# Optimization experiments

Hardware: AMD Instinct MI355X
Metric: run time of the kernel (lower is better)

The kernel has to match this reference:

```python
import jax, jax.numpy as jnp
import numpy as np

N_MEL = 80
ATTN = 512
PRENET = 256
RNN = 1024
B, T = 32, 800


def setup_inputs() -> dict:
    key = jax.random.key(0)
    ks = jax.random.split(key, 10)
    s = lambda fan_in: 1.0 / np.sqrt(fan_in)
    return {
        "memory": jax.random.normal(ks[0], (B, T, ATTN), jnp.float32),
        "y_mels": jax.random.normal(ks[1], (B, T, N_MEL), jnp.float32),
        # Prenet: two bias-free linears with ReLU
        "prenet_w1": jax.random.uniform(ks[2], (PRENET, N_MEL), jnp.float32, -s(N_MEL), s(N_MEL)),
        "prenet_w2": jax.random.uniform(ks[3], (PRENET, PRENET), jnp.float32, -s(PRENET), s(PRENET)),
        # LSTM (1 layer): input dim = PRENET + ATTN = 768, gate order i,f,g,o
        "w_ih": jax.random.uniform(ks[4], (4 * RNN, PRENET + ATTN), jnp.float32, -s(RNN), s(RNN)),
        "w_hh": jax.random.uniform(ks[5], (4 * RNN, RNN), jnp.float32, -s(RNN), s(RNN)),
        "b_ih": jax.random.uniform(ks[6], (4 * RNN,), jnp.float32, -s(RNN), s(RNN)),
        "b_hh": jax.random.uniform(ks[7], (4 * RNN,), jnp.float32, -s(RNN), s(RNN)),
        # Linear projection: (RNN + ATTN) -> N_MEL, with bias
        "proj_w": jax.random.uniform(ks[8], (N_MEL, RNN + ATTN), jnp.float32, -s(RNN + ATTN), s(RNN + ATTN)),
        "proj_b": jax.random.uniform(ks[9], (N_MEL,), jnp.float32, -s(RNN + ATTN), s(RNN + ATTN)),
    }


def _decoder_fwd(memory, y_mels, prenet_w1, prenet_w2, w_ih, w_hh, b_ih, b_hh, proj_w, proj_b):
    b, t, _ = memory.shape
    # teacher-forced previous frames: step j consumes zeros (j=0) or y_mels[:, j-1]
    prev = jnp.concatenate([jnp.zeros((b, 1, N_MEL), memory.dtype), y_mels[:, : t - 1]], axis=1)  # [B,T,80]
    # prenet (eval mode: dropout off; double relu == relu)
    h = jax.nn.relu(jnp.einsum("btm,pm->btp", prev, prenet_w1))
    h = jax.nn.relu(jnp.einsum("btp,qp->btq", h, prenet_w2))  # [B,T,256]
    x = jnp.concatenate([h, memory], axis=-1)  # [B,T,768]
    # precompute input-to-gate contributions for all steps
    gates_in = jnp.einsum("btd,gd->tbg", x, w_ih) + (b_ih + b_hh)  # [T,B,4H]

    def step(carry, g_in):
        hh, cc = carry
        gates = g_in + hh @ w_hh.T  # [B,4H]
        i, f_, g, o = jnp.split(gates, 4, axis=-1)
        cc = jax.nn.sigmoid(f_) * cc + jax.nn.sigmoid(i) * jnp.tanh(g)
        hh = jax.nn.sigmoid(o) * jnp.tanh(cc)
        return (hh, cc), hh

    init = (jnp.zeros((b, RNN), memory.dtype), jnp.zeros((b, RNN), memory.dtype))
    _, hs = jax.lax.scan(step, init, gates_in)  # [T,B,H]
    hs = jnp.transpose(hs, (1, 0, 2))  # [B,T,H]
    out = jnp.concatenate([hs, memory], axis=-1)  # [B,T,H+ATTN]
    mel = jnp.einsum("btd,md->btm", out, proj_w) + proj_b  # [B,T,80]
    return mel.reshape(b, -1, N_MEL)


def reference(memory, y_mels, prenet_w1, prenet_w2, w_ih, w_hh, b_ih, b_hh, proj_w, proj_b):
    return _decoder_fwd(memory, y_mels, prenet_w1, prenet_w2, w_ih, w_hh, b_ih, b_hh, proj_w, proj_b)
```

## Files before the change

### kernel.cpp

```cpp
#include <hip/hip_runtime.h>
#include <hip/hip_bf16.h>

typedef unsigned short u16;
typedef unsigned int u32;
typedef unsigned long long u64;
typedef __attribute__((ext_vector_type(8))) short short8;
typedef __attribute__((ext_vector_type(4))) float f32x4;
typedef __attribute__((ext_vector_type(4))) u32 u32x4;

#define ROWS 25600

__device__ __forceinline__ u16 f2bf(float f){
  u32 x = __builtin_bit_cast(u32, f);
  u32 r = (x + 0x7FFFu + ((x >> 16) & 1u)) >> 16;
  return (u16)r;
}
__device__ __forceinline__ float bf2f(u16 h){
  return __builtin_bit_cast(float, ((u32)h) << 16);
}
__device__ __forceinline__ float sigf(float x){
  x = fminf(fmaxf(x, -30.f), 30.f);
  return 1.f / (1.f + __expf(-x));
}
__device__ __forceinline__ float tanh_(float x){
  x = fminf(fmaxf(x, -15.f), 15.f);
  float e = __expf(-2.f * x);
  return (1.f - e) / (1.f + e);
}


__global__ void initk(u32* wflags, u32* pflags, u16* hb){
  int i = blockIdx.x * blockDim.x + threadIdx.x;
  int stride = blockDim.x * gridDim.x;
  for (int j = i; j < 64 * 32; j += stride) wflags[j] = 0;
  for (int j = i; j < 192 * 32; j += stride) pflags[j] = 0;
  for (int j = i; j < 2 * 32 * 1024; j += stride) hb[j] = 0;
}

__global__ void sentinel_fill(float* out, int n, float val){
  for (int i = blockIdx.x * blockDim.x + threadIdx.x; i < n;
       i += blockDim.x * gridDim.x)
    out[i] = val;
}

__global__ void prep_prev(const float* __restrict__ ym, u16* __restrict__ prevp){
  int idx = blockIdx.x * blockDim.x + threadIdx.x;
  if (idx >= ROWS * 96) return;
  int r = idx / 96, c = idx - r * 96;
  int b = r / 800, t = r - b * 800;
  float v = 0.f;
  if (c < 80 && t > 0) v = ym[(u64)(b * 800 + (t - 1)) * 80 + c];
  prevp[idx] = f2bf(v);
}

__global__ void prep_w(const float* __restrict__ w1, const float* __restrict__ w2,
                       const float* __restrict__ wih, const float* __restrict__ pw,
                       const float* __restrict__ bih, const float* __restrict__ bhh,
                       const float* __restrict__ whh,
                       u16* __restrict__ w1p, u16* __restrict__ w2b,
                       u16* __restrict__ wihb, u16* __restrict__ projp,
                       float* __restrict__ bsum, u16* __restrict__ whhb){
  int idx = blockIdx.x * blockDim.x + threadIdx.x;
  const int n1 = 256 * 96, n2 = 256 * 256, n3 = 4096 * 768, n4 = 128 * 1536, n5 = 4096;
  const int n6 = 4096 * 1024;
  if (idx < n1){
    int r = idx / 96, c = idx - r * 96;
    w1p[idx] = (c < 80) ? f2bf(w1[r * 80 + c]) : (u16)0;
  } else if ((idx -= n1) < n2){
    w2b[idx] = f2bf(w2[idx]);
  } else if ((idx -= n2) < n3){
    wihb[idx] = f2bf(wih[idx]);
  } else if ((idx -= n3) < n4){
    int r = idx / 1536;
    projp[idx] = (r < 80) ? f2bf(pw[idx]) : (u16)0;
  } else if ((idx -= n4) < n5){
    bsum[idx] = bih[idx] + bhh[idx];
  } else if ((idx -= n5) < n6){
    whhb[idx] = f2bf(whh[idx]);
  }
}


template<int RELU, int OUTF32, int HASBIAS, int AMAP, int SPLIT>
__global__ __launch_bounds__(256, 2) void gemm_tn(
    const u16* __restrict__ A, const float* __restrict__ A2,
    const u16* __restrict__ W, void* __restrict__ Cv,
    const float* __restrict__ bias,
    int M, int K, int lda, int lda2, int ldw, int ldc, int nmax,
    int ksplit, int t0)
{
  __shared__ __align__(16) u16 As[128 * 32];
  __shared__ __align__(16) u16 Ws[128 * 32];
  const int tid = threadIdx.x;
  const int lane = tid & 63;
  const int wv = tid >> 6;
  const int wr = wv & 1, wc = wv >> 1;
  const int mtiles = M >> 7;
  const int ntiles = gridDim.x / mtiles;
  int bm, bn;
  if (mtiles & 7){
    bm = blockIdx.x % mtiles;
    bn = blockIdx.x / mtiles;
  } else {
    int per = 8 * ntiles;
    int g = blockIdx.x / per, rem = blockIdx.x % per;
    bm = g * 8 + (rem & 7);
    bn = rem >> 3;
  }
  const int m0 = bm << 7, n0 = bn << 7;
  const int KT = K >> 5;

  f32x4 acc[4][4] = {};

  const int r0 = tid >> 2, c0 = tid & 3;
  const int r1 = r0 + 64;
  const u16* Wb = W + (u64)n0 * ldw;
  const int ws0 = r0 * 32 + ((c0 ^ ((r0 >> 1) & 3)) << 3);
  const int ws1 = r1 * 32 + ((c0 ^ ((r1 >> 1) & 3)) << 3);

  auto rowmap = [&](int r) -> int {
    int gr = m0 + r;
    if (AMAP) return (gr & 31) * 800 + t0 + (gr >> 5);
    return gr;
  };
  const u64 ab0 = (u64)rowmap(r0) * lda;
  const u64 ab1 = (u64)rowmap(r1) * lda;
  const u64 af0 = SPLIT ? (u64)rowmap(r0) * lda2 : 0;
  const u64 af1 = SPLIT ? (u64)rowmap(r1) * lda2 : 0;

  auto aload = [&](u64 rb, u64 rf, int k) -> uint4 {
    if (SPLIT && k >= ksplit){
      const float* p = A2 + rf + (k - ksplit);
      const float4 a = *(const float4*)p;
      const float4 b = *(const float4*)(p + 4);
      uint4 r;
      r.x = (u32)f2bf(a.x) | ((u32)f2bf(a.y) << 16);
      r.y = (u32)f2bf(a.z) | ((u32)f2bf(a.w) << 16);
      r.z = (u32)f2bf(b.x) | ((u32)f2bf(b.y) << 16);
      r.w = (u32)f2bf(b.z) | ((u32)f2bf(b.w) << 16);
      return r;
    }
    return *(const uint4*)(A + rb + k);
  };

  uint4 ra0 = aload(ab0, af0, c0 * 8);
  uint4 ra1 = aload(ab1, af1, c0 * 8);
  uint4 rw0 = *(const uint4*)(Wb + r0 * ldw + c0 * 8);
  uint4 rw1 = *(const uint4*)(Wb + r1 * ldw + c0 * 8);

  const int r16 = lane & 15, cg = lane >> 4;

  for (int kt = 0; kt < KT; ++kt){
    *(uint4*)&As[ws0] = ra0;
    *(uint4*)&As[ws1] = ra1;
    *(uint4*)&Ws[ws0] = rw0;
    *(uint4*)&Ws[ws1] = rw1;
    __syncthreads();
    if (kt + 1 < KT){
      const int k0 = ((kt + 1) << 5) + c0 * 8;
      ra0 = aload(ab0, af0, k0);
      ra1 = aload(ab1, af1, k0);
      rw0 = *(const uint4*)(Wb + r0 * ldw + k0);
      rw1 = *(const uint4*)(Wb + r1 * ldw + k0);
    }
    short8 af[4], wf[4];
    #pragma unroll
    for (int mt = 0; mt < 4; ++mt){
      const int row = (wr << 6) + (mt << 4) + r16;
      af[mt] = *(const short8*)&As[(row << 5) + ((cg ^ ((row >> 1) & 3)) << 3)];
    }
    #pragma unroll
    for (int nt = 0; nt < 4; ++nt){
      const int row = (wc << 6) + (nt << 4) + r16;
      wf[nt] = *(const short8*)&Ws[(row << 5) + ((cg ^ ((row >> 1) & 3)) << 3)];
    }
    #pragma unroll
    for (int mt = 0; mt < 4; ++mt)
      #pragma unroll
      for (int nt = 0; nt < 4; ++nt)
        acc[mt][nt] = __builtin_amdgcn_mfma_f32_16x16x32_bf16(af[mt], wf[nt], acc[mt][nt], 0, 0, 0);
    __syncthreads();
  }

  #pragma unroll
  for (int nt = 0; nt < 4; ++nt){
    const int gn = n0 + (wc << 6) + (nt << 4) + r16;
    if (gn < nmax){
      float bv = 0.f;
      if (HASBIAS) bv = bias[gn];
      #pragma unroll
      for (int mt = 0; mt < 4; ++mt){
        #pragma unroll
        for (int r = 0; r < 4; ++r){
          const int gm = m0 + (wr << 6) + (mt << 4) + (cg << 2) + r;
          float v = acc[mt][nt][r] + bv;
          if (RELU) v = fmaxf(v, 0.f);
          if (OUTF32) ((float*)Cv)[(u64)gm * ldc + gn] = v;
          else        ((u16*)Cv)[(u64)gm * ldc + gn] = f2bf(v);
        }
      }
    }
  }
}


__shared__ __align__(16) u16 fs_hsm[32 * 1024];
__shared__ __align__(16) float fs_gsm[2048];
__shared__ __align__(16) u16 fs_As[128 * 32];
__shared__ __align__(16) u16 fs_Ws[128 * 32];

__device__ void gemm_tile_512(
    const u16* __restrict__ pn, const float* __restrict__ memory,
    const u16* __restrict__ wihb, const float* __restrict__ bsum,
    u16* __restrict__ slot, int bm, int bn, int t0)
{
  const int tid = threadIdx.x;
  const bool act = (tid < 256);
  const int lane = tid & 63;
  const int wv4 = (tid >> 6) & 3;
  const int wr = wv4 & 1, wc = wv4 >> 1;
  const int m0 = bm << 7, n0 = bn << 7;
  const int KT = 24;

  f32x4 acc[4][4] = {};
  const int r0 = tid >> 2, c0 = tid & 3;
  const int r1 = r0 + 64;
  const u16* Wb = wihb + (u64)n0 * 768;
  const int ws0 = r0 * 32 + ((c0 ^ ((r0 >> 1) & 3)) << 3);
  const int ws1 = r1 * 32 + ((c0 ^ ((r1 >> 1) & 3)) << 3);

  auto rowmap = [&](int r) -> int {
    int gr = m0 + r;
    return (gr & 31) * 800 + t0 + (gr >> 5);
  };
  u64 ab0 = 0, ab1 = 0, af0 = 0, af1 = 0;
  if (act){
    ab0 = (u64)rowmap(r0) * 256;  af0 = (u64)rowmap(r0) * 512;
    ab1 = (u64)rowmap(r1) * 256;  af1 = (u64)rowmap(r1) * 512;
  }
  auto aload = [&](u64 rb, u64 rf, int k) -> uint4 {
    if (k >= 256){
      const float* p = memory + rf + (k - 256);
      const float4 a = *(const float4*)p;
      const float4 b = *(const float4*)(p + 4);
      uint4 r;
      r.x = (u32)f2bf(a.x) | ((u32)f2bf(a.y) << 16);
      r.y = (u32)f2bf(a.z) | ((u32)f2bf(a.w) << 16);
      r.z = (u32)f2bf(b.x) | ((u32)f2bf(b.y) << 16);
      r.w = (u32)f2bf(b.z) | ((u32)f2bf(b.w) << 16);
      return r;
    }
    return *(const uint4*)(pn + rb + k);
  };

  uint4 ra0, ra1, rw0, rw1;
  if (act){
    ra0 = aload(ab0, af0, c0 * 8);
    ra1 = aload(ab1, af1, c0 * 8);
    rw0 = *(const uint4*)(Wb + r0 * 768 + c0 * 8);
    rw1 = *(const uint4*)(Wb + r1 * 768 + c0 * 8);
  }
  const int r16 = lane & 15, cg = lane >> 4;

  for (int kt = 0; kt < KT; ++kt){
    if (act){
      *(uint4*)&fs_As[ws0] = ra0;
      *(uint4*)&fs_As[ws1] = ra1;
      *(uint4*)&fs_Ws[ws0] = rw0;
      *(uint4*)&fs_Ws[ws1] = rw1;
    }
    __syncthreads();
    if (act){
      if (kt + 1 < KT){
        const int k0 = ((kt + 1) << 5) + c0 * 8;
        ra0 = aload(ab0, af0, k0);
        ra1 = aload(ab1, af1, k0);
        rw0 = *(const uint4*)(Wb + r0 * 768 + k0);
        rw1 = *(const uint4*)(Wb + r1 * 768 + k0);
      }
      short8 af[4], wf[4];
      #pragma unroll
      for (int mt = 0; mt < 4; ++mt){
        const int row = (wr << 6) + (mt << 4) + r16;
        af[mt] = *(const short8*)&fs_As[(row << 5) + ((cg ^ ((row >> 1) & 3)) << 3)];
      }
      #pragma unroll
      for (int nt = 0; nt < 4; ++nt){
        const int row = (wc << 6) + (nt << 4) + r16;
        wf[nt] = *(const short8*)&fs_Ws[(row << 5) + ((cg ^ ((row >> 1) & 3)) << 3)];
      }
      #pragma unroll
      for (int mt = 0; mt < 4; ++mt)
        #pragma unroll
        for (int nt = 0; nt < 4; ++nt)
          acc[mt][nt] = __builtin_amdgcn_mfma_f32_16x16x32_bf16(af[mt], wf[nt], acc[mt][nt], 0, 0, 0);
    }
    __syncthreads();
  }

  if (act){
    #pragma unroll
    for (int nt = 0; nt < 4; ++nt){
      const int gn = n0 + (wc << 6) + (nt << 4) + r16;
      const float bv = bsum[gn];
      #pragma unroll
      for (int mt = 0; mt < 4; ++mt){
        #pragma unroll
        for (int r = 0; r < 4; ++r){
          const int gm = m0 + (wr << 6) + (mt << 4) + (cg << 2) + r;
          slot[(u64)gm * 4096 + gn] = f2bf(acc[mt][nt][r] + bv);
        }
      }
    }
  }
}

__global__ __launch_bounds__(512, 1) void fused(
    const u16* __restrict__ whhb, const u16* __restrict__ pn,
    const float* __restrict__ memory, const u16* __restrict__ wihb,
    const float* __restrict__ bsum, u16* __restrict__ ring,
    u16* __restrict__ hb, u16* __restrict__ hs,
    u32* wflags, u32* pflags, int CT, int nchunks)
{
  const int tid = threadIdx.x;
  const int lane = tid & 63;
  const int wv = tid >> 6;
  const u64 deadline = __builtin_amdgcn_s_memrealtime() + 100000000ull;

  if (blockIdx.x >= 64){
    const int p = blockIdx.x - 64;
    for (int c = 0; c < nchunks; ++c){
      const int t0 = c * CT;
      const int steps = (800 - t0 < CT) ? (800 - t0) : CT;
      if (c >= 2){
        if (wv == 0){
          const u32 need = (u32)((c - 1) * CT);
          u32 it = 0;
          while (1){
            u32 v = __hip_atomic_load(&wflags[lane << 5], __ATOMIC_RELAXED,
                                      __HIP_MEMORY_SCOPE_AGENT);
            if (__all((int)(v >= need))) break;
            __builtin_amdgcn_s_sleep(8);
            if (((++it) & 15u) == 0u &&
                __builtin_amdgcn_s_memrealtime() > deadline) break;
          }
        }
        __syncthreads();
      }
      const int mt = (steps * 32) >> 7;
      const int TPC = mt * 32;
      u16* slot = ring + (u64)(c & 1) * ((u64)CT << 17);
      for (int tau = p; tau < TPC; tau += 192){
        gemm_tile_512(pn, memory, wihb, bsum, slot, tau % mt, tau / mt, t0);
      }
      __syncthreads();
      if (wv == 0){
        __builtin_amdgcn_fence(__ATOMIC_RELEASE, "agent");
        if (tid == 0)
          __hip_atomic_store(&pflags[p << 5], (u32)(c + 1), __ATOMIC_RELAXED,
                             __HIP_MEMORY_SCOPE_AGENT);
      }
    }
    return;
  }

  const int gate = wv & 3, mh = wv >> 2;
  const int u0 = blockIdx.x << 4;
  const int r16 = lane & 15, cg = lane >> 4;

  short8 wf[32];
  {
    const u16* wrow = whhb + (u64)((gate << 10) + u0 + r16) * 1024 + (cg << 3);
    #pragma unroll
    for (int kk = 0; kk < 32; ++kk)
      wf[kk] = *(const short8*)(wrow + (kk << 5));
    #pragma unroll
    for (int kk = 0; kk < 32; ++kk)
      asm volatile("" : "+v"(wf[kk]));
  }

  const int pb = tid >> 4, pu = tid & 15;
  float ccell = 0.f;
  const int arow = (mh << 4) + r16;
  const u16* abase = &fs_hsm[arow << 10];
  const int aswz = (arow & 7) << 3;

  int c = 0, i = 0;
  for (int t = 0; t < 800; ++t, ++i){
    if (i == CT){ c++; i = 0; }
    const bool boundary = (i == 0);
    const u16* gslot = ring + (u64)(c & 1) * ((u64)CT << 17);
    const u64 gb = ((u64)i * 32 + pb) * 4096 + u0 + pu;
    const int cur = t & 1;

    u16 gv0 = 0, gv1 = 0, gv2 = 0, gv3 = 0;
    if (!boundary){
      gv0 = gslot[gb];        gv1 = gslot[gb + 1024];
      gv2 = gslot[gb + 2048]; gv3 = gslot[gb + 3072];
    }
    if (boundary || t > 0){
      if (wv == 0){
        if (boundary){
          const u32 need = (u32)(c + 1);
          u32 it = 0;
          while (1){
            u32 a = __hip_atomic_load(&pflags[lane << 5], __ATOMIC_RELAXED,
                                      __HIP_MEMORY_SCOPE_AGENT);
            u32 b = __hip_atomic_load(&pflags[(lane + 64) << 5], __ATOMIC_RELAXED,
                                      __HIP_MEMORY_SCOPE_AGENT);
            u32 d = __hip_atomic_load(&pflags[(lane + 128) << 5], __ATOMIC_RELAXED,
                                      __HIP_MEMORY_SCOPE_AGENT);
            u32 m = a < b ? a : b; m = m < d ? m : d;
            if (__all((int)(m >= need))) break;
            if (((++it) & 15u) == 0u &&
                __builtin_amdgcn_s_memrealtime() > deadline) break;
          }
        }
        if (t > 0){
          u32 it = 0;
          while (1){
            u32 v = __hip_atomic_load(&wflags[lane << 5], __ATOMIC_RELAXED,
                                      __HIP_MEMORY_SCOPE_AGENT);
            if (__all((int)(v >= (u32)t))) break;
            if (((++it) & 15u) == 0u &&
                __builtin_amdgcn_s_memrealtime() > deadline) break;
          }
        }
        if (boundary)
          __builtin_amdgcn_fence(__ATOMIC_ACQUIRE, "agent");
      }
      __syncthreads();
    }
    if (boundary){
      gv0 = gslot[gb];        gv1 = gslot[gb + 1024];
      gv2 = gslot[gb + 2048]; gv3 = gslot[gb + 3072];
    }
    {
      const u16* hsrc = hb + cur * 32768;
      u32x4 hr[8];
      {
        u32x4 h0,h1,h2,h3,h4,h5,h6,h7;
        const u32 ob = (u32)tid << 4;
        asm volatile(
          "global_load_dwordx4 %0, %8, %16 sc0 sc1\n\t"
          "global_load_dwordx4 %1, %9, %16 sc0 sc1\n\t"
          "global_load_dwordx4 %2, %10, %16 sc0 sc1\n\t"
          "global_load_dwordx4 %3, %11, %16 sc0 sc1\n\t"
          "global_load_dwordx4 %4, %12, %16 sc0 sc1\n\t"
          "global_load_dwordx4 %5, %13, %16 sc0 sc1\n\t"
          "global_load_dwordx4 %6, %14, %16 sc0 sc1\n\t"
          "global_load_dwordx4 %7, %15, %16 sc0 sc1\n\t"
          "s_waitcnt vmcnt(0)"
          : "=&v"(h0), "=&v"(h1), "=&v"(h2), "=&v"(h3),
            "=&v"(h4), "=&v"(h5), "=&v"(h6), "=&v"(h7)
          : "v"(ob), "v"(ob + 8192u), "v"(ob + 16384u), "v"(ob + 24576u),
            "v"(ob + 32768u), "v"(ob + 40960u), "v"(ob + 49152u), "v"(ob + 57344u),
            "s"(hsrc)
          : "memory");
        __builtin_amdgcn_sched_barrier(0);
        hr[0]=h0; hr[1]=h1; hr[2]=h2; hr[3]=h3;
        hr[4]=h4; hr[5]=h5; hr[6]=h6; hr[7]=h7;
      }
      #pragma unroll
      for (int j = 0; j < 8; ++j){
        const int ci = (j << 9) + tid;
        const int row = ci >> 7, k16 = ci & 127;
        *(u32x4*)&fs_hsm[(row << 10) + ((k16 ^ (row & 7)) << 3)] = hr[j];
      }
    }
    __syncthreads();
    f32x4 acc = {};
    #pragma unroll
    for (int kk = 0; kk < 32; ++kk){
      const int k16 = (kk << 2) + cg;
      const short8 af = *(const short8*)&abase[((k16 << 3) ^ aswz)];
      acc = __builtin_amdgcn_mfma_f32_16x16x32_bf16(af, wf[kk], acc, 0, 0, 0);
    }
    #pragma unroll
    for (int r = 0; r < 4; ++r){
      const int m = (mh << 4) + (cg << 2) + r;
      fs_gsm[(gate << 9) + (m << 4) + r16] = acc[r];
    }
    __syncthreads();
    u16 hbits;
    {
      const int o = (pb << 4) + pu;
      const float gi = fs_gsm[o]        + bf2f(gv0);
      const float gf = fs_gsm[512 + o]  + bf2f(gv1);
      const float gg = fs_gsm[1024 + o] + bf2f(gv2);
      const float go = fs_gsm[1536 + o] + bf2f(gv3);
      ccell = sigf(gf) * ccell + sigf(gi) * tanh_(gg);
      const float h = sigf(go) * tanh_(ccell);
      hbits = f2bf(h);
      const u32 other = (u32)(u16)__shfl_xor((int)(u32)hbits, 1);
      if ((tid & 1) == 0){
        const u32 w = ((u32)hbits) | (other << 16);
        u32* dst = (u32*)(void*)hb + ((cur ^ 1) * 16384 + (pb << 9) + (u0 >> 1) + (pu >> 1));
        __hip_atomic_store(dst, w, __ATOMIC_RELAXED, __HIP_MEMORY_SCOPE_AGENT);
      }
    }
    __syncthreads();
    if (tid == 0)
      __hip_atomic_store(&wflags[blockIdx.x << 5], (u32)(t + 1), __ATOMIC_RELAXED,
                         __HIP_MEMORY_SCOPE_AGENT);
    hs[(((u64)pb * 800 + t) << 10) + u0 + pu] = hbits;
  }
}


extern "C" void kernel_launch(void* const* d_in, const int* in_sizes, int n_in,
                              void* d_out, int out_size, void* d_ws, size_t ws_size,
                              hipStream_t stream){
  const float* memory = (const float*)d_in[0];
  const float* ymels  = (const float*)d_in[1];
  const float* w1     = (const float*)d_in[2];
  const float* w2     = (const float*)d_in[3];
  const float* wih    = (const float*)d_in[4];
  const float* whh    = (const float*)d_in[5];
  const float* bih    = (const float*)d_in[6];
  const float* bhh    = (const float*)d_in[7];
  const float* pw     = (const float*)d_in[8];
  const float* pbias  = (const float*)d_in[9];
  float* out = (float*)d_out;

  char* ws = (char*)d_ws;
  u64 off = 0;
  auto alloc = [&](u64 bytes) -> void* {
    void* p = ws + off;
    off += (bytes + 255) & ~255ull;
    return p;
  };
  u16* hs    = (u16*)alloc((u64)ROWS * 1024 * 2);
  u16* pn    = (u16*)alloc((u64)ROWS * 256 * 2);
  u16* wihb  = (u16*)alloc((u64)4096 * 768 * 2);
  u16* whhb  = (u16*)alloc((u64)4096 * 1024 * 2);
  u16* w1p   = (u16*)alloc(256 * 96 * 2);
  u16* w2b   = (u16*)alloc(256 * 256 * 2);
  u16* projp = (u16*)alloc(128 * 1536 * 2);
  float* bsum = (float*)alloc(4096 * 4);
  u16* hb    = (u16*)alloc(2 * 32768 * 2);
  u32* wflags = (u32*)alloc(64 * 32 * 4);
  u32* pflags = (u32*)alloc(192 * 32 * 4);
  u16* prevp = hs;
  u16* h1b   = hs + (8u << 20);

  int CT = 0;
  u16* ring = (u16*)(ws + off);
  if (ws_size > off){
    u64 avail = ws_size - off;
    CT = (int)(avail / (2ull * 32 * 4096 * 2));
    CT &= ~3;
    if (CT > 64) CT = 64;
  }
  if (CT < 8){
    float val = 1.0e6f + 10.0f * (float)(ws_size >> 20);
    sentinel_fill<<<256, 256, 0, stream>>>(out, out_size, val);
    return;
  }
  const int nchunks = (800 + CT - 1) / CT;

  initk<<<64, 256, 0, stream>>>(wflags, pflags, hb);
  prep_prev<<<(ROWS * 96) / 256, 256, 0, stream>>>(ymels, prevp);
  prep_w<<<(256*96 + 256*256 + 4096*768 + 128*1536 + 4096 + 4096*1024 + 255) / 256,
           256, 0, stream>>>(
      w1, w2, wih, pw, bih, bhh, whh, w1p, w2b, wihb, projp, bsum, whhb);

  gemm_tn<1,0,0,0,0><<<200 * 2, 256, 0, stream>>>(prevp, nullptr, w1p, h1b, nullptr,
      ROWS, 96, 96, 0, 96, 256, 256, 0, 0);
  gemm_tn<1,0,0,0,0><<<200 * 2, 256, 0, stream>>>(h1b, nullptr, w2b, pn, nullptr,
      ROWS, 256, 256, 0, 256, 256, 256, 0, 0);

  fused<<<256, 512, 0, stream>>>(whhb, pn, memory, wihb, bsum, ring, hb, hs,
                                 wflags, pflags, CT, nchunks);

  gemm_tn<0,1,1,0,1><<<200 * 1, 256, 0, stream>>>(hs, memory, projp, out, pbias,
      ROWS, 1536, 1024, 512, 1536, 80, 80, 1024, 0);
}
```

Measured before the change: 2.895 ms.

## Replace per-step flag barrier with poison-polled per-timestep hidden-state buffer

The hidden state is now written to a per-timestep buffer (801 slots) pre-filled with a NaN poison pattern. Consumers spin on the data until no poisoned words remain, which replaces the per-step wflags store and the wait that went with it, and drops the extra hs write. The projection GEMM reads the step-major buffer directly through new row-remap template flags. The cost is a larger workspace, a big poison init, and a reliance on relaxed stores landing atomically per dword. A real hidden value that happens to match the poison pattern would also stall the spin.

```diff
diff --git a/kernel.cpp b/kernel.cpp
--- a/kernel.cpp
+++ b/kernel.cpp
@@ -9,6 +9,7 @@
 typedef __attribute__((ext_vector_type(4))) u32 u32x4;
 
 #define ROWS 25600
+#define POISON 0x7FC07FC0u
 
 __device__ __forceinline__ u16 f2bf(float f){
   u32 x = __builtin_bit_cast(u32, f);
@@ -29,12 +30,14 @@
 }
 
 
-__global__ void initk(u32* wflags, u32* pflags, u16* hb){
+__global__ void initk(u32* wflags, u32* pflags, u32* hstep){
   int i = blockIdx.x * blockDim.x + threadIdx.x;
   int stride = blockDim.x * gridDim.x;
   for (int j = i; j < 64 * 32; j += stride) wflags[j] = 0;
   for (int j = i; j < 192 * 32; j += stride) pflags[j] = 0;
-  for (int j = i; j < 2 * 32 * 1024; j += stride) hb[j] = 0;
+  const int total = 801 * 16384;
+  for (int j = i; j < total; j += stride)
+    hstep[j] = (j < 16384) ? 0u : POISON;
 }
 
 __global__ void sentinel_fill(float* out, int n, float val){
@@ -81,7 +84,7 @@
 }
 
 
-template<int RELU, int OUTF32, int HASBIAS, int AMAP, int SPLIT>
+template<int RELU, int OUTF32, int HASBIAS, int AMAP, int A2MAP, int OMAP, int SPLIT>
 __global__ __launch_bounds__(256, 2) void gemm_tn(
     const u16* __restrict__ A, const float* __restrict__ A2,
     const u16* __restrict__ W, void* __restrict__ Cv,
@@ -118,15 +121,14 @@
   const int ws0 = r0 * 32 + ((c0 ^ ((r0 >> 1) & 3)) << 3);
   const int ws1 = r1 * 32 + ((c0 ^ ((r1 >> 1) & 3)) << 3);
 
-  auto rowmap = [&](int r) -> int {
+  auto maprow = [&](int r) -> int {
     int gr = m0 + r;
-    if (AMAP) return (gr & 31) * 800 + t0 + (gr >> 5);
-    return gr;
+    return (gr & 31) * 800 + t0 + (gr >> 5);
   };
-  const u64 ab0 = (u64)rowmap(r0) * lda;
-  const u64 ab1 = (u64)rowmap(r1) * lda;
-  const u64 af0 = SPLIT ? (u64)rowmap(r0) * lda2 : 0;
-  const u64 af1 = SPLIT ? (u64)rowmap(r1) * lda2 : 0;
+  const u64 ab0 = (u64)(AMAP  ? maprow(r0) : m0 + r0) * lda;
+  const u64 ab1 = (u64)(AMAP  ? maprow(r1) : m0 + r1) * lda;
+  const u64 af0 = SPLIT ? (u64)(A2MAP ? maprow(r0) : m0 + r0) * lda2 : 0;
+  const u64 af1 = SPLIT ? (u64)(A2MAP ? maprow(r1) : m0 + r1) * lda2 : 0;
 
   auto aload = [&](u64 rb, u64 rf, int k) -> uint4 {
     if (SPLIT && k >= ksplit){
@@ -195,8 +197,9 @@
           const int gm = m0 + (wr << 6) + (mt << 4) + (cg << 2) + r;
           float v = acc[mt][nt][r] + bv;
           if (RELU) v = fmaxf(v, 0.f);
-          if (OUTF32) ((float*)Cv)[(u64)gm * ldc + gn] = v;
-          else        ((u16*)Cv)[(u64)gm * ldc + gn] = f2bf(v);
+          const int orow = OMAP ? ((gm & 31) * 800 + t0 + (gm >> 5)) : gm;
+          if (OUTF32) ((float*)Cv)[(u64)orow * ldc + gn] = v;
+          else        ((u16*)Cv)[(u64)orow * ldc + gn] = f2bf(v);
         }
       }
     }
@@ -319,8 +322,7 @@
     const u16* __restrict__ whhb, const u16* __restrict__ pn,
     const float* __restrict__ memory, const u16* __restrict__ wihb,
     const float* __restrict__ bsum, u16* __restrict__ ring,
-    u16* __restrict__ hb, u16* __restrict__ hs,
-    u32* wflags, u32* pflags, int CT, int nchunks)
+    u16* __restrict__ hstep, u32* wflags, u32* pflags, int CT, int nchunks)
 {
   const int tid = threadIdx.x;
   const int lane = tid & 63;
@@ -334,7 +336,7 @@
       const int steps = (800 - t0 < CT) ? (800 - t0) : CT;
       if (c >= 2){
         if (wv == 0){
-          const u32 need = (u32)((c - 1) * CT);
+          const u32 need = (u32)(c - 1);
           u32 it = 0;
           while (1){
             u32 v = __hip_atomic_load(&wflags[lane << 5], __ATOMIC_RELAXED,
@@ -391,56 +393,43 @@
     const bool boundary = (i == 0);
     const u16* gslot = ring + (u64)(c & 1) * ((u64)CT << 17);
     const u64 gb = ((u64)i * 32 + pb) * 4096 + u0 + pu;
-    const int cur = t & 1;
 
     u16 gv0 = 0, gv1 = 0, gv2 = 0, gv3 = 0;
     if (!boundary){
       gv0 = gslot[gb];        gv1 = gslot[gb + 1024];
       gv2 = gslot[gb + 2048]; gv3 = gslot[gb + 3072];
     }
-    if (boundary || t > 0){
+    if (boundary){
       if (wv == 0){
-        if (boundary){
-          const u32 need = (u32)(c + 1);
-          u32 it = 0;
-          while (1){
-            u32 a = __hip_atomic_load(&pflags[lane << 5], __ATOMIC_RELAXED,
-                                      __HIP_MEMORY_SCOPE_AGENT);
-            u32 b = __hip_atomic_load(&pflags[(lane + 64) << 5], __ATOMIC_RELAXED,
-                                      __HIP_MEMORY_SCOPE_AGENT);
-            u32 d = __hip_atomic_load(&pflags[(lane + 128) << 5], __ATOMIC_RELAXED,
-                                      __HIP_MEMORY_SCOPE_AGENT);
-            u32 m = a < b ? a : b; m = m < d ? m : d;
-            if (__all((int)(m >= need))) break;
-            if (((++it) & 15u) == 0u &&
-                __builtin_amdgcn_s_memrealtime() > deadline) break;
-          }
+        if (lane == 0)
+          __hip_atomic_store(&wflags[blockIdx.x << 5], (u32)c, __ATOMIC_RELAXED,
+                             __HIP_MEMORY_SCOPE_AGENT);
+        const u32 need = (u32)(c + 1);
+        u32 it = 0;
+        while (1){
+          u32 a = __hip_atomic_load(&pflags[lane << 5], __ATOMIC_RELAXED,
+                                    __HIP_MEMORY_SCOPE_AGENT);
+          u32 b = __hip_atomic_load(&pflags[(lane + 64) << 5], __ATOMIC_RELAXED,
+                                    __HIP_MEMORY_SCOPE_AGENT);
+          u32 d = __hip_atomic_load(&pflags[(lane + 128) << 5], __ATOMIC_RELAXED,
+                                    __HIP_MEMORY_SCOPE_AGENT);
+          u32 m = a < b ? a : b; m = m < d ? m : d;
+          if (__all((int)(m >= need))) break;
+          if (((++it) & 15u) == 0u &&
+              __builtin_amdgcn_s_memrealtime() > deadline) break;
         }
-        if (t > 0){
-          u32 it = 0;
-          while (1){
-            u32 v = __hip_atomic_load(&wflags[lane << 5], __ATOMIC_RELAXED,
-                                      __HIP_MEMORY_SCOPE_AGENT);
-            if (__all((int)(v >= (u32)t))) break;
-            if (((++it) & 15u) == 0u &&
-                __builtin_amdgcn_s_memrealtime() > deadline) break;
-          }
-        }
-        if (boundary)
-          __builtin_amdgcn_fence(__ATOMIC_ACQUIRE, "agent");
+        __builtin_amdgcn_fence(__ATOMIC_ACQUIRE, "agent");
       }
       __syncthreads();
-    }
-    if (boundary){
       gv0 = gslot[gb];        gv1 = gslot[gb + 1024];
       gv2 = gslot[gb + 2048]; gv3 = gslot[gb + 3072];
     }
+    u32x4 hr0, hr1, hr2, hr3, hr4, hr5, hr6, hr7;
     {
-      const u16* hsrc = hb + cur * 32768;
-      u32x4 hr[8];
-      {
-        u32x4 h0,h1,h2,h3,h4,h5,h6,h7;
-        const u32 ob = (u32)tid << 4;
+      const u16* hsrc = hstep + (u64)t * 32768;
+      const u32 ob = (u32)tid << 4;
+      u32 attempts = 0;
+      while (1){
         asm volatile(
           "global_load_dwordx4 %0, %8, %16 sc0 sc1\n\t"
           "global_load_dwordx4 %1, %9, %16 sc0 sc1\n\t"
@@ -451,16 +440,27 @@
           "global_load_dwordx4 %6, %14, %16 sc0 sc1\n\t"
           "global_load_dwordx4 %7, %15, %16 sc0 sc1\n\t"
           "s_waitcnt vmcnt(0)"
-          : "=&v"(h0), "=&v"(h1), "=&v"(h2), "=&v"(h3),
-            "=&v"(h4), "=&v"(h5), "=&v"(h6), "=&v"(h7)
+          : "=&v"(hr0), "=&v"(hr1), "=&v"(hr2), "=&v"(hr3),
+            "=&v"(hr4), "=&v"(hr5), "=&v"(hr6), "=&v"(hr7)
           : "v"(ob), "v"(ob + 8192u), "v"(ob + 16384u), "v"(ob + 24576u),
             "v"(ob + 32768u), "v"(ob + 40960u), "v"(ob + 49152u), "v"(ob + 57344u),
             "s"(hsrc)
           : "memory");
-        __builtin_amdgcn_sched_barrier(0);
-        hr[0]=h0; hr[1]=h1; hr[2]=h2; hr[3]=h3;
-        hr[4]=h4; hr[5]=h5; hr[6]=h6; hr[7]=h7;
-      }
+        bool ok = true;
+        #pragma unroll
+        for (int e = 0; e < 4; ++e){
+          ok &= (hr0[e] != POISON); ok &= (hr1[e] != POISON);
+          ok &= (hr2[e] != POISON); ok &= (hr3[e] != POISON);
+          ok &= (hr4[e] != POISON); ok &= (hr5[e] != POISON);
+          ok &= (hr6[e] != POISON); ok &= (hr7[e] != POISON);
+        }
+        if (ok) break;
+        if (((++attempts) & 15u) == 0u &&
+            __builtin_amdgcn_s_memrealtime() > deadline) break;
+      }
+    }
+    {
+      u32x4 hr[8] = {hr0, hr1, hr2, hr3, hr4, hr5, hr6, hr7};
       #pragma unroll
       for (int j = 0; j < 8; ++j){
         const int ci = (j << 9) + tid;
@@ -482,7 +482,6 @@
       fs_gsm[(gate << 9) + (m << 4) + r16] = acc[r];
     }
     __syncthreads();
-    u16 hbits;
     {
       const int o = (pb << 4) + pu;
       const float gi = fs_gsm[o]        + bf2f(gv0);
@@ -491,19 +490,15 @@
       const float go = fs_gsm[1536 + o] + bf2f(gv3);
       ccell = sigf(gf) * ccell + sigf(gi) * tanh_(gg);
       const float h = sigf(go) * tanh_(ccell);
-      hbits = f2bf(h);
+      const u16 hbits = f2bf(h);
       const u32 other = (u32)(u16)__shfl_xor((int)(u32)hbits, 1);
       if ((tid & 1) == 0){
         const u32 w = ((u32)hbits) | (other << 16);
-        u32* dst = (u32*)(void*)hb + ((cur ^ 1) * 16384 + (pb << 9) + (u0 >> 1) + (pu >> 1));
+        u32* dst = (u32*)(void*)hstep +
+                   ((u64)(t + 1) * 16384 + (pb << 9) + (u0 >> 1) + (pu >> 1));
         __hip_atomic_store(dst, w, __ATOMIC_RELAXED, __HIP_MEMORY_SCOPE_AGENT);
       }
     }
-    __syncthreads();
-    if (tid == 0)
-      __hip_atomic_store(&wflags[blockIdx.x << 5], (u32)(t + 1), __ATOMIC_RELAXED,
-                         __HIP_MEMORY_SCOPE_AGENT);
-    hs[(((u64)pb * 800 + t) << 10) + u0 + pu] = hbits;
   }
 }
 
@@ -530,7 +525,7 @@
     off += (bytes + 255) & ~255ull;
     return p;
   };
-  u16* hs    = (u16*)alloc((u64)ROWS * 1024 * 2);
+  u16* hstep = (u16*)alloc((u64)801 * 32768 * 2);
   u16* pn    = (u16*)alloc((u64)ROWS * 256 * 2);
   u16* wihb  = (u16*)alloc((u64)4096 * 768 * 2);
   u16* whhb  = (u16*)alloc((u64)4096 * 1024 * 2);
@@ -538,11 +533,10 @@
   u16* w2b   = (u16*)alloc(256 * 256 * 2);
   u16* projp = (u16*)alloc(128 * 1536 * 2);
   float* bsum = (float*)alloc(4096 * 4);
-  u16* hb    = (u16*)alloc(2 * 32768 * 2);
   u32* wflags = (u32*)alloc(64 * 32 * 4);
   u32* pflags = (u32*)alloc(192 * 32 * 4);
-  u16* prevp = hs;
-  u16* h1b   = hs + (8u << 20);
+  u16* prevp = (u16*)alloc((u64)ROWS * 96 * 2);
+  u16* h1b   = (u16*)alloc((u64)ROWS * 256 * 2);
 
   int CT = 0;
   u16* ring = (u16*)(ws + off);
@@ -559,20 +553,20 @@
   }
   const int nchunks = (800 + CT - 1) / CT;
 
-  initk<<<64, 256, 0, stream>>>(wflags, pflags, hb);
+  initk<<<256, 256, 0, stream>>>(wflags, pflags, (u32*)(void*)hstep);
   prep_prev<<<(ROWS * 96) / 256, 256, 0, stream>>>(ymels, prevp);
   prep_w<<<(256*96 + 256*256 + 4096*768 + 128*1536 + 4096 + 4096*1024 + 255) / 256,
            256, 0, stream>>>(
       w1, w2, wih, pw, bih, bhh, whh, w1p, w2b, wihb, projp, bsum, whhb);
 
-  gemm_tn<1,0,0,0,0><<<200 * 2, 256, 0, stream>>>(prevp, nullptr, w1p, h1b, nullptr,
+  gemm_tn<1,0,0,0,0,0,0><<<200 * 2, 256, 0, stream>>>(prevp, nullptr, w1p, h1b, nullptr,
       ROWS, 96, 96, 0, 96, 256, 256, 0, 0);
-  gemm_tn<1,0,0,0,0><<<200 * 2, 256, 0, stream>>>(h1b, nullptr, w2b, pn, nullptr,
+  gemm_tn<1,0,0,0,0,0,0><<<200 * 2, 256, 0, stream>>>(h1b, nullptr, w2b, pn, nullptr,
       ROWS, 256, 256, 0, 256, 256, 256, 0, 0);
 
-  fused<<<256, 512, 0, stream>>>(whhb, pn, memory, wihb, bsum, ring, hb, hs,
-                                 wflags, pflags, CT, nchunks);
-
-  gemm_tn<0,1,1,0,1><<<200 * 1, 256, 0, stream>>>(hs, memory, projp, out, pbias,
-      ROWS, 1536, 1024, 512, 1536, 80, 80, 1024, 0);
-}
+  fused<<<256, 512, 0, stream>>>(whhb, pn, memory, wihb, bsum, ring,
+                                 hstep, wflags, pflags, CT, nchunks);
+
+  gemm_tn<0,1,1,0,1,1,1><<<200 * 1, 256, 0, stream>>>(hstep + 32768, memory, projp,
+      out, pbias, ROWS, 1536, 1024, 512, 1536, 80, 80, 1024, 0);
+}
```

New measurement: 4.229 ms. 1.46x slower.
